# Optimization experiments

Measured on AMD Instinct MI355X. Metric: run time of the kernel, lower is better.

The kernel has to match this reference:

```python
import jax, jax.numpy as jnp
import numpy as np

N, C, H, W = 4, 64, 64, 64
K = 3


def _unfold(x, k):
    """torch F.unfold with padding k//2: [n,c,h,w] -> [n, c*k*k, h*w].
    Feature ordering matches torch: index = c*k*k + i*k + j."""
    p = k // 2
    n, c, h, w = x.shape
    xp = jnp.pad(x, ((0, 0), (0, 0), (p, p), (p, p)))
    patches = jnp.stack(
        [xp[:, :, i:i + h, j:j + w] for i in range(k) for j in range(k)], axis=2
    )  # [n, c, k*k, h, w]
    return patches.reshape(n, c * k * k, h * w)


def _mask_vec(c, k):
    # causal patch mask from __init__: zero out center-and-right of middle row and all rows below
    m = np.ones((c, k, k), np.float32)
    m[:, k // 2, k // 2:] = 0
    m[:, k // 2 + 1:, :] = 0
    return jnp.asarray(m.reshape(1, c * k * k, 1))


def setup_inputs() -> dict:
    key = jax.random.key(0)
    k1, k2 = jax.random.split(key)
    y_hat = jax.random.normal(k1, (N, C, H, W), dtype=jnp.float32)
    y_prob = jax.random.uniform(k2, (N, 1, H, W), dtype=jnp.float32)
    return {"y_hat": y_hat, "y_prob": y_prob}


def reference(y_hat, y_prob):
    k = K
    n, c, h, w = y_hat.shape
    L = h * w
    mask = _mask_vec(c, k)

    u = _unfold(y_hat, k) * mask                              # [n, c*k*k, L]
    u = u / jnp.maximum(jnp.linalg.norm(u, axis=1, keepdims=True), 1e-12)
    R = jnp.einsum('nfl,nfm->nlm', u, u)                      # [n, L, L] cosine sims

    # eval path: keep strictly-upper triangle (causal: l < m)
    row = jnp.arange(L)[:, None]
    col = jnp.arange(L)[None, :]
    R = jnp.where(col > row, R, 0.0)

    R_star = jnp.max(R, axis=1)                               # [n, L]
    arg = jnp.argmax(R, axis=1).astype(jnp.int32)             # [n, L]

    y_unf = _unfold(y_hat, k)                                 # [n, c*k*k, L]
    ref_unfold = jnp.take_along_axis(y_unf, arg[:, None, :], axis=2)

    prob_unf = y_prob.reshape(n, -1, L)                       # 1x1 unfold
    U_unf = jnp.take_along_axis(prob_unf, arg[:, None, :], axis=2)

    S = R_star.reshape(n, 1, h, w)
    U = U_unf.reshape(n, -1, h, w)

    # eval-mode position-0 overrides
    S = S.at[:, :, 0, 0].set(1e-8)
    U = U.at[:, :, 0, 0].set(1e-8)
    ref_unfold = ref_unfold.at[:, :, 0].set(0.0)
    arg = arg.at[:, 0].set(-1)

    S = jnp.clip(S, 1e-8, 1.0)
    U = jnp.clip(U, 1e-8, 1.0)
    return S, U, ref_unfold, arg
```

## Files before the change

### kernel.cpp

```cpp
#include <hip/hip_runtime.h>
#include <stdint.h>

#define Nn 4
#define Cc 64
#define LL 4096
#define KK 256
#define NB 32
#define TRI2 528
#define PAD_H 40

typedef _Float16 half8 __attribute__((ext_vector_type(8)));
typedef float f32x4 __attribute__((ext_vector_type(4)));

__device__ __forceinline__ unsigned f2ord(float f) {
    unsigned u = __float_as_uint(f);
    return u ^ ((u & 0x80000000u) ? 0xFFFFFFFFu : 0x80000000u);
}
__device__ __forceinline__ float ord2f(unsigned o) {
    unsigned u = (o & 0x80000000u) ? (o ^ 0x80000000u) : ~o;
    return __uint_as_float(u);
}
__device__ __forceinline__ unsigned short h2u(_Float16 h) {
    union { _Float16 f; unsigned short u; } x; x.f = h; return x.u;
}

__global__ __launch_bounds__(256) void build_v(const float* __restrict__ yhat,
                                               unsigned short* __restrict__ VhT,
                                               unsigned short* __restrict__ VlT) {
    int gid = blockIdx.x * 256 + threadIdx.x;
    int cg = gid & 7;
    int nl = gid >> 3;
    int n = nl >> 12;
    int l = nl & (LL - 1);
    int y = l >> 6, x = l & 63;
    const float* src = yhat + (size_t)n * (Cc * LL);

    float vals[32];
    float sumsq = 0.f;
#pragma unroll
    for (int ci = 0; ci < 8; ++ci) {
        const float* p = src + (cg * 8 + ci) * LL;
        float t0 = (y > 0 && x > 0)  ? p[l - 65] : 0.f;
        float t1 = (y > 0)           ? p[l - 64] : 0.f;
        float t2 = (y > 0 && x < 63) ? p[l - 63] : 0.f;
        float t3 = (x > 0)           ? p[l - 1]  : 0.f;
        vals[ci * 4 + 0] = t0; vals[ci * 4 + 1] = t1;
        vals[ci * 4 + 2] = t2; vals[ci * 4 + 3] = t3;
        sumsq += t0 * t0 + t1 * t1 + t2 * t2 + t3 * t3;
    }
    sumsq += __shfl_xor(sumsq, 1, 64);
    sumsq += __shfl_xor(sumsq, 2, 64);
    sumsq += __shfl_xor(sumsq, 4, 64);
    float inv = 1.f / fmaxf(sqrtf(sumsq), 1e-12f);

    unsigned short* dh = VhT + (size_t)nl * KK + cg * 32;
    unsigned short* dl = VlT + (size_t)nl * KK + cg * 32;
#pragma unroll
    for (int ci = 0; ci < 8; ++ci) {
        ushort4 hv, lv;
        unsigned short* ph = &hv.x;
        unsigned short* pl = &lv.x;
#pragma unroll
        for (int tp = 0; tp < 4; ++tp) {
            float v = vals[ci * 4 + tp] * inv;
            _Float16 h = (fabsf(v) < 6.1035e-5f) ? (_Float16)0 : (_Float16)v;
            _Float16 lo = (_Float16)((v - (float)h) * 2048.0f);
            ph[tp] = h2u(h);
            pl[tp] = h2u(lo);
        }
        *(ushort4*)(dh + ci * 4) = hv;
        *(ushort4*)(dl + ci * 4) = lv;
    }
}

__global__ __launch_bounds__(256) void simmax(const unsigned short* __restrict__ Vh,
                                              const unsigned short* __restrict__ Vl,
                                              unsigned long long* __restrict__ best) {
    __shared__ __align__(16) unsigned short Ah[128 * PAD_H];
    __shared__ __align__(16) unsigned short Al[128 * PAD_H];
    __shared__ __align__(16) unsigned short Bh[128 * PAD_H];
    __shared__ __align__(16) unsigned short Bl[128 * PAD_H];

    int bx = blockIdx.x;
    int n = bx / TRI2;
    int t = bx % TRI2;
    int j = (int)((sqrtf(8.f * (float)t + 1.f) - 1.f) * 0.5f);
    while ((j + 1) * (j + 2) / 2 <= t) ++j;
    while (j * (j + 1) / 2 > t) --j;
    int i = t - j * (j + 1) / 2;
    int l0 = i * 128, m0 = j * 128;

    const unsigned short* VhB = Vh + (size_t)n * (LL * KK);
    const unsigned short* VlB = Vl + (size_t)n * (LL * KK);

    int tid = threadIdx.x;
    int w = tid >> 6, lane = tid & 63;
    int quad = lane >> 4, l16 = lane & 15;
    int rw = (w & 1) * 64;
    int cw = (w >> 1) * 64;
    bool skip = (i == j) && (rw == 64) && (cw == 0);

    f32x4 acc[4][4];
#pragma unroll
    for (int r = 0; r < 4; ++r)
#pragma unroll
        for (int c = 0; c < 4; ++c) acc[r][c] = (f32x4)0.f;

    int srow = tid >> 2;
    int sh = (tid & 3) * 8;

    for (int k0 = 0; k0 < KK; k0 += 32) {
        const size_t ra = (size_t)(l0 + srow) * KK + k0 + sh;
        const size_t rb = (size_t)(l0 + 64 + srow) * KK + k0 + sh;
        const size_t rc = (size_t)(m0 + srow) * KK + k0 + sh;
        const size_t rd = (size_t)(m0 + 64 + srow) * KK + k0 + sh;
        uint4 ah0 = *(const uint4*)(VhB + ra);
        uint4 ah1 = *(const uint4*)(VhB + rb);
        uint4 al0 = *(const uint4*)(VlB + ra);
        uint4 al1 = *(const uint4*)(VlB + rb);
        uint4 bh0 = *(const uint4*)(VhB + rc);
        uint4 bh1 = *(const uint4*)(VhB + rd);
        uint4 bl0 = *(const uint4*)(VlB + rc);
        uint4 bl1 = *(const uint4*)(VlB + rd);
        __syncthreads();
        *(uint4*)&Ah[srow * PAD_H + sh]        = ah0;
        *(uint4*)&Ah[(64 + srow) * PAD_H + sh] = ah1;
        *(uint4*)&Al[srow * PAD_H + sh]        = al0;
        *(uint4*)&Al[(64 + srow) * PAD_H + sh] = al1;
        *(uint4*)&Bh[srow * PAD_H + sh]        = bh0;
        *(uint4*)&Bh[(64 + srow) * PAD_H + sh] = bh1;
        *(uint4*)&Bl[srow * PAD_H + sh]        = bl0;
        *(uint4*)&Bl[(64 + srow) * PAD_H + sh] = bl1;
        __syncthreads();
        if (!skip) {
            half8 ah[4], al[4], bh[4], bl[4];
#pragma unroll
            for (int r = 0; r < 4; ++r) {
                ah[r] = *(half8*)&Ah[(rw + r * 16 + l16) * PAD_H + quad * 8];
                al[r] = *(half8*)&Al[(rw + r * 16 + l16) * PAD_H + quad * 8];
                bh[r] = *(half8*)&Bh[(cw + r * 16 + l16) * PAD_H + quad * 8];
                bl[r] = *(half8*)&Bl[(cw + r * 16 + l16) * PAD_H + quad * 8];
            }
#pragma unroll
            for (int r = 0; r < 4; ++r)
#pragma unroll
                for (int c = 0; c < 4; ++c)
                    acc[r][c] = __builtin_amdgcn_mfma_f32_16x16x32_f16(al[r], bh[c], acc[r][c], 0, 0, 0);
#pragma unroll
            for (int r = 0; r < 4; ++r)
#pragma unroll
                for (int c = 0; c < 4; ++c)
                    acc[r][c] = __builtin_amdgcn_mfma_f32_16x16x32_f16(ah[r], bl[c], acc[r][c], 0, 0, 0);
#pragma unroll
            for (int r = 0; r < 4; ++r)
#pragma unroll
                for (int q = 0; q < 8; ++q) ah[r][q] = ah[r][q] * (_Float16)2048.0f;
#pragma unroll
            for (int r = 0; r < 4; ++r)
#pragma unroll
                for (int c = 0; c < 4; ++c)
                    acc[r][c] = __builtin_amdgcn_mfma_f32_16x16x32_f16(ah[r], bh[c], acc[r][c], 0, 0, 0);
        }
    }

    if (skip) return;
    unsigned long long* bb = best + (size_t)n * LL;
    const float s = 1.f / 2048.f;
#pragma unroll
    for (int c = 0; c < 4; ++c) {
        int m = m0 + cw + c * 16 + l16;
        unsigned long long key = 0ull;
#pragma unroll
        for (int r = 0; r < 4; ++r)
#pragma unroll
            for (int g = 0; g < 4; ++g) {
                int l = l0 + rw + r * 16 + quad * 4 + g;
                if (l < m) {
                    float v = acc[r][c][g] * s;
                    unsigned long long k2 =
                        ((unsigned long long)f2ord(v) << 32) |
                        (unsigned long long)(0xFFFFFFFFu - (unsigned)l);
                    key = (k2 > key) ? k2 : key;
                }
            }
        unsigned long long o1 = __shfl_xor(key, 16, 64); key = (o1 > key) ? o1 : key;
        unsigned long long o2 = __shfl_xor(key, 32, 64); key = (o2 > key) ? o2 : key;
        if (quad == 0 && key != 0ull) atomicMax(bb + m, key);
    }
}

__global__ __launch_bounds__(256) void writeout(const float* __restrict__ yhat,
                                                const float* __restrict__ yprob,
                                                const unsigned long long* __restrict__ best,
                                                float* __restrict__ out) {
    int bx = blockIdx.x;
    int n = bx >> 8;
    int mb = (bx >> 2) & 63;
    int fc = bx & 3;
    int tid = threadIdx.x;
    int mm = tid & 63;
    int fs = tid >> 6;
    int m = mb * 64 + mm;

    unsigned long long key = best[(size_t)n * LL + m];
    unsigned l = 0xFFFFFFFFu - (unsigned)(key & 0xFFFFFFFFull);
    float val = ord2f((unsigned)(key >> 32));
    bool zero = (m == 0);
    if (zero) l = 0;
    int ly = (int)(l >> 6), lx = (int)(l & 63);

    float* Sout = out;
    float* Uout = out + 16384;
    float* Rout = out + 32768;
    float* Aout = out + 9469952;

    if (fc == 0 && fs == 0) {
        float S = zero ? 1e-8f : fminf(fmaxf(val, 1e-8f), 1.0f);
        float U = zero ? 1e-8f : fminf(fmaxf(yprob[(size_t)n * LL + l], 1e-8f), 1.0f);
        Sout[(size_t)n * LL + m] = S;
        Uout[(size_t)n * LL + m] = U;
        Aout[(size_t)n * LL + m] = zero ? -1.0f : (float)l;
    }

    const float* src = yhat + (size_t)n * (Cc * LL);
    float* dst = Rout + (size_t)n * (576 * LL) + m;
#pragma unroll 4
    for (int ii = 0; ii < 36; ++ii) {
        int f = fc * 144 + fs + 4 * ii;
        int c = f / 9, ij = f % 9;
        int di = ij / 3 - 1, dj = ij % 3 - 1;
        int yy = ly + di, xx = lx + dj;
        float v = 0.f;
        if (!zero && yy >= 0 && yy < 64 && xx >= 0 && xx < 64)
            v = src[(size_t)c * LL + yy * 64 + xx];
        dst[(size_t)f * LL] = v;
    }
}

extern "C" void kernel_launch(void* const* d_in, const int* in_sizes, int n_in,
                              void* d_out, int out_size, void* d_ws, size_t ws_size,
                              hipStream_t stream) {
    const float* yhat  = (const float*)d_in[0];
    const float* yprob = (const float*)d_in[1];
    float* out = (float*)d_out;

    unsigned short* VhT = (unsigned short*)d_ws;
    unsigned short* VlT = (unsigned short*)((char*)d_ws + 8388608);
    unsigned long long* best =
        (unsigned long long*)((char*)d_ws + 16777216);

    hipMemsetAsync(best, 0, (size_t)Nn * LL * sizeof(unsigned long long), stream);
    build_v<<<512, 256, 0, stream>>>(yhat, VhT, VlT);
    simmax<<<Nn * TRI2, 256, 0, stream>>>(VhT, VlT, best);
    writeout<<<Nn * 64 * 4, 256, 0, stream>>>(yhat, yprob, best, out);
}
```

Measured before the change: 165.9 us.

## Switch simmax to 32x32 MFMA, prescale hi part, remap blocks per XCD, vectorize writeout

The similarity kernel moves from 16x16x32 to 32x32x16 f16 MFMA tiles, with the epilogue row mapping and lane reduction rewritten to match. The high half is stored pre-multiplied by 2048, which removes the in-loop rescale. Blocks are remapped so each XCD handles one batch half, to improve L2 locality. build_v uses twice as many threads with fewer channels each, and writeout loads 3-wide rows as unaligned vectors and uses nontemporal stores. Together these aim to cut LDS/register overhead, improve cache reuse and speed up the gather/store phase, at the risk of fp16 range issues from the prescaled values.

```diff
diff --git a/kernel.cpp b/kernel.cpp
--- a/kernel.cpp
+++ b/kernel.cpp
@@ -10,7 +10,8 @@
 #define PAD_H 40
 
 typedef _Float16 half8 __attribute__((ext_vector_type(8)));
-typedef float f32x4 __attribute__((ext_vector_type(4)));
+typedef float f32x16 __attribute__((ext_vector_type(16)));
+typedef float f4a __attribute__((ext_vector_type(4), aligned(4)));
 
 __device__ __forceinline__ unsigned f2ord(float f) {
     unsigned u = __float_as_uint(f);
@@ -28,18 +29,18 @@
                                                unsigned short* __restrict__ VhT,
                                                unsigned short* __restrict__ VlT) {
     int gid = blockIdx.x * 256 + threadIdx.x;
-    int cg = gid & 7;
-    int nl = gid >> 3;
+    int cg = gid & 15;
+    int nl = gid >> 4;
+    int l = nl & (LL - 1);
     int n = nl >> 12;
-    int l = nl & (LL - 1);
     int y = l >> 6, x = l & 63;
     const float* src = yhat + (size_t)n * (Cc * LL);
 
-    float vals[32];
+    float vals[16];
     float sumsq = 0.f;
 #pragma unroll
-    for (int ci = 0; ci < 8; ++ci) {
-        const float* p = src + (cg * 8 + ci) * LL;
+    for (int ci = 0; ci < 4; ++ci) {
+        const float* p = src + (cg * 4 + ci) * LL;
         float t0 = (y > 0 && x > 0)  ? p[l - 65] : 0.f;
         float t1 = (y > 0)           ? p[l - 64] : 0.f;
         float t2 = (y > 0 && x < 63) ? p[l - 63] : 0.f;
@@ -51,12 +52,13 @@
     sumsq += __shfl_xor(sumsq, 1, 64);
     sumsq += __shfl_xor(sumsq, 2, 64);
     sumsq += __shfl_xor(sumsq, 4, 64);
+    sumsq += __shfl_xor(sumsq, 8, 64);
     float inv = 1.f / fmaxf(sqrtf(sumsq), 1e-12f);
 
-    unsigned short* dh = VhT + (size_t)nl * KK + cg * 32;
-    unsigned short* dl = VlT + (size_t)nl * KK + cg * 32;
-#pragma unroll
-    for (int ci = 0; ci < 8; ++ci) {
+    unsigned short* dh = VhT + (size_t)nl * KK + cg * 16;
+    unsigned short* dl = VlT + (size_t)nl * KK + cg * 16;
+#pragma unroll
+    for (int ci = 0; ci < 4; ++ci) {
         ushort4 hv, lv;
         unsigned short* ph = &hv.x;
         unsigned short* pl = &lv.x;
@@ -65,7 +67,7 @@
             float v = vals[ci * 4 + tp] * inv;
             _Float16 h = (fabsf(v) < 6.1035e-5f) ? (_Float16)0 : (_Float16)v;
             _Float16 lo = (_Float16)((v - (float)h) * 2048.0f);
-            ph[tp] = h2u(h);
+            ph[tp] = h2u(h * (_Float16)2048.0f);
             pl[tp] = h2u(lo);
         }
         *(ushort4*)(dh + ci * 4) = hv;
@@ -82,8 +84,9 @@
     __shared__ __align__(16) unsigned short Bl[128 * PAD_H];
 
     int bx = blockIdx.x;
-    int n = bx / TRI2;
-    int t = bx % TRI2;
+    int xcd = bx & 7, idx = bx >> 3;
+    int n = xcd >> 1;
+    int t = (xcd & 1) * 264 + idx;
     int j = (int)((sqrtf(8.f * (float)t + 1.f) - 1.f) * 0.5f);
     while ((j + 1) * (j + 2) / 2 <= t) ++j;
     while (j * (j + 1) / 2 > t) --j;
@@ -95,16 +98,16 @@
 
     int tid = threadIdx.x;
     int w = tid >> 6, lane = tid & 63;
-    int quad = lane >> 4, l16 = lane & 15;
+    int r5 = lane & 31, h5 = lane >> 5;
     int rw = (w & 1) * 64;
     int cw = (w >> 1) * 64;
     bool skip = (i == j) && (rw == 64) && (cw == 0);
 
-    f32x4 acc[4][4];
-#pragma unroll
-    for (int r = 0; r < 4; ++r)
-#pragma unroll
-        for (int c = 0; c < 4; ++c) acc[r][c] = (f32x4)0.f;
+    f32x16 acc[2][2];
+#pragma unroll
+    for (int r = 0; r < 2; ++r)
+#pragma unroll
+        for (int c = 0; c < 2; ++c) acc[r][c] = (f32x16)0.f;
 
     int srow = tid >> 2;
     int sh = (tid & 3) * 8;
@@ -133,48 +136,54 @@
         *(uint4*)&Bl[(64 + srow) * PAD_H + sh] = bl1;
         __syncthreads();
         if (!skip) {
-            half8 ah[4], al[4], bh[4], bl[4];
-#pragma unroll
-            for (int r = 0; r < 4; ++r) {
-                ah[r] = *(half8*)&Ah[(rw + r * 16 + l16) * PAD_H + quad * 8];
-                al[r] = *(half8*)&Al[(rw + r * 16 + l16) * PAD_H + quad * 8];
-                bh[r] = *(half8*)&Bh[(cw + r * 16 + l16) * PAD_H + quad * 8];
-                bl[r] = *(half8*)&Bl[(cw + r * 16 + l16) * PAD_H + quad * 8];
-            }
-#pragma unroll
-            for (int r = 0; r < 4; ++r)
-#pragma unroll
-                for (int c = 0; c < 4; ++c)
-                    acc[r][c] = __builtin_amdgcn_mfma_f32_16x16x32_f16(al[r], bh[c], acc[r][c], 0, 0, 0);
-#pragma unroll
-            for (int r = 0; r < 4; ++r)
-#pragma unroll
-                for (int c = 0; c < 4; ++c)
-                    acc[r][c] = __builtin_amdgcn_mfma_f32_16x16x32_f16(ah[r], bl[c], acc[r][c], 0, 0, 0);
-#pragma unroll
-            for (int r = 0; r < 4; ++r)
-#pragma unroll
-                for (int q = 0; q < 8; ++q) ah[r][q] = ah[r][q] * (_Float16)2048.0f;
-#pragma unroll
-            for (int r = 0; r < 4; ++r)
-#pragma unroll
-                for (int c = 0; c < 4; ++c)
-                    acc[r][c] = __builtin_amdgcn_mfma_f32_16x16x32_f16(ah[r], bh[c], acc[r][c], 0, 0, 0);
+            half8 fah[2][2], fal[2][2], fbh[2][2], fbl[2][2];
+#pragma unroll
+            for (int r = 0; r < 2; ++r)
+#pragma unroll
+                for (int kc = 0; kc < 2; ++kc) {
+                    int ao = (rw + r * 32 + r5) * PAD_H + kc * 16 + h5 * 8;
+                    int bo = (cw + r * 32 + r5) * PAD_H + kc * 16 + h5 * 8;
+                    fah[r][kc] = *(half8*)&Ah[ao];
+                    fal[r][kc] = *(half8*)&Al[ao];
+                    fbh[r][kc] = *(half8*)&Bh[bo];
+                    fbl[r][kc] = *(half8*)&Bl[bo];
+                }
+#pragma unroll
+            for (int kc = 0; kc < 2; ++kc)
+#pragma unroll
+                for (int r = 0; r < 2; ++r)
+#pragma unroll
+                    for (int c = 0; c < 2; ++c)
+                        acc[r][c] = __builtin_amdgcn_mfma_f32_32x32x16_f16(fal[r][kc], fbh[c][kc], acc[r][c], 0, 0, 0);
+#pragma unroll
+            for (int kc = 0; kc < 2; ++kc)
+#pragma unroll
+                for (int r = 0; r < 2; ++r)
+#pragma unroll
+                    for (int c = 0; c < 2; ++c)
+                        acc[r][c] = __builtin_amdgcn_mfma_f32_32x32x16_f16(fah[r][kc], fbl[c][kc], acc[r][c], 0, 0, 0);
+#pragma unroll
+            for (int kc = 0; kc < 2; ++kc)
+#pragma unroll
+                for (int r = 0; r < 2; ++r)
+#pragma unroll
+                    for (int c = 0; c < 2; ++c)
+                        acc[r][c] = __builtin_amdgcn_mfma_f32_32x32x16_f16(fah[r][kc], fbh[c][kc], acc[r][c], 0, 0, 0);
         }
     }
 
     if (skip) return;
     unsigned long long* bb = best + (size_t)n * LL;
-    const float s = 1.f / 2048.f;
-#pragma unroll
-    for (int c = 0; c < 4; ++c) {
-        int m = m0 + cw + c * 16 + l16;
+    const float s = 1.f / 4194304.f;
+#pragma unroll
+    for (int c = 0; c < 2; ++c) {
+        int m = m0 + cw + c * 32 + r5;
         unsigned long long key = 0ull;
 #pragma unroll
-        for (int r = 0; r < 4; ++r)
-#pragma unroll
-            for (int g = 0; g < 4; ++g) {
-                int l = l0 + rw + r * 16 + quad * 4 + g;
+        for (int r = 0; r < 2; ++r)
+#pragma unroll
+            for (int g = 0; g < 16; ++g) {
+                int l = l0 + rw + r * 32 + (g & 3) + 8 * (g >> 2) + 4 * h5;
                 if (l < m) {
                     float v = acc[r][c][g] * s;
                     unsigned long long k2 =
@@ -183,9 +192,9 @@
                     key = (k2 > key) ? k2 : key;
                 }
             }
-        unsigned long long o1 = __shfl_xor(key, 16, 64); key = (o1 > key) ? o1 : key;
-        unsigned long long o2 = __shfl_xor(key, 32, 64); key = (o2 > key) ? o2 : key;
-        if (quad == 0 && key != 0ull) atomicMax(bb + m, key);
+        unsigned long long o = __shfl_xor(key, 32, 64);
+        key = (o > key) ? o : key;
+        if (h5 == 0 && key != 0ull) atomicMax(bb + m, key);
     }
 }
 
@@ -224,16 +233,31 @@
 
     const float* src = yhat + (size_t)n * (Cc * LL);
     float* dst = Rout + (size_t)n * (576 * LL) + m;
-#pragma unroll 4
-    for (int ii = 0; ii < 36; ++ii) {
-        int f = fc * 144 + fs + 4 * ii;
-        int c = f / 9, ij = f % 9;
-        int di = ij / 3 - 1, dj = ij % 3 - 1;
-        int yy = ly + di, xx = lx + dj;
-        float v = 0.f;
-        if (!zero && yy >= 0 && yy < 64 && xx >= 0 && xx < 64)
-            v = src[(size_t)c * LL + yy * 64 + xx];
-        dst[(size_t)f * LL] = v;
+    bool fast = (!zero) && (lx >= 1) && (lx <= 61);
+#pragma unroll
+    for (int cc = 0; cc < 4; ++cc) {
+        int c = fc * 16 + fs * 4 + cc;
+        const float* plane = src + (size_t)c * LL;
+#pragma unroll
+        for (int r3 = 0; r3 < 3; ++r3) {
+            int yy = ly + r3 - 1;
+            bool rowok = (!zero) && (yy >= 0) && (yy < 64);
+            float t0 = 0.f, t1 = 0.f, t2 = 0.f;
+            if (rowok) {
+                if (fast) {
+                    f4a v = *(const f4a*)(plane + yy * 64 + lx - 1);
+                    t0 = v.x; t1 = v.y; t2 = v.z;
+                } else {
+                    if (lx > 0)  t0 = plane[yy * 64 + lx - 1];
+                    t1 = plane[yy * 64 + lx];
+                    if (lx < 63) t2 = plane[yy * 64 + lx + 1];
+                }
+            }
+            size_t f = (size_t)(c * 9 + r3 * 3) * LL;
+            __builtin_nontemporal_store(t0, dst + f);
+            __builtin_nontemporal_store(t1, dst + f + LL);
+            __builtin_nontemporal_store(t2, dst + f + 2 * (size_t)LL);
+        }
     }
 }
 
@@ -250,7 +274,7 @@
         (unsigned long long*)((char*)d_ws + 16777216);
 
     hipMemsetAsync(best, 0, (size_t)Nn * LL * sizeof(unsigned long long), stream);
-    build_v<<<512, 256, 0, stream>>>(yhat, VhT, VlT);
+    build_v<<<1024, 256, 0, stream>>>(yhat, VhT, VlT);
     simmax<<<Nn * TRI2, 256, 0, stream>>>(VhT, VlT, best);
     writeout<<<Nn * 64 * 4, 256, 0, stream>>>(yhat, yprob, best, out);
 }
```

Result: no change. 162.8 us (-1.9%).
